# Optimization experiments

Measured on AMD Instinct MI355X. Metric: run time of the kernel, lower is better.

Reference implementation:

```python
import jax, jax.numpy as jnp
import numpy as np

B, S, C_MEL, D_MODEL, K, MAX_DUR = 4, 128, 80, 256, 9, 16
EPS = 1e-5


def setup_inputs():
    key = jax.random.key(0)
    ks = jax.random.split(key, 8)
    rng = np.random.RandomState(0)
    duration = rng.randint(4, MAX_DUR, size=(B, S)).astype(np.int32)
    mel_len = duration.sum(axis=1).astype(np.int32)
    M = int(mel_len.max())
    H = D_MODEL
    def nrm(k, shape, s=0.05):
        return jax.random.normal(k, shape, jnp.float32) * s
    return {
        'mel': jax.random.normal(ks[0], (B, M, C_MEL), jnp.float32),
        'mel_len': jnp.asarray(mel_len),
        'duration': jnp.asarray(duration),
        'src_len': jnp.full((B,), S, dtype=jnp.int32),
        'max_dur': MAX_DUR,
        'conv1_w': nrm(ks[1], (1, K, 1, H), 0.1),
        'bn1_gamma': jnp.ones((H,), jnp.float32),
        'bn1_beta': jnp.zeros((H,), jnp.float32),
        'conv2_w': nrm(ks[2], (1, K, H, 1), 0.05),
        'bn2_gamma': jnp.ones((1,), jnp.float32),
        'bn2_beta': jnp.zeros((1,), jnp.float32),
        'w_ih_f': nrm(ks[3], (3 * H, C_MEL)),
        'w_hh_f': nrm(ks[4], (3 * H, H)),
        'b_ih_f': jnp.zeros((3 * H,), jnp.float32),
        'b_hh_f': jnp.zeros((3 * H,), jnp.float32),
        'w_ih_b': nrm(ks[5], (3 * H, C_MEL)),
        'w_hh_b': nrm(ks[6], (3 * H, H)),
        'b_ih_b': jnp.zeros((3 * H,), jnp.float32),
        'b_hh_b': jnp.zeros((3 * H,), jnp.float32),
    }


def _conv_block(x, w, gamma, beta):
    # x: [N, H=n_mel, W=time, Cin]; conv kernel (1, K) along time, SAME pad, no bias
    p = (w.shape[1] - 1) // 2
    y = jax.lax.conv_general_dilated(x, w, (1, 1), ((0, 0), (p, p)),
                                     dimension_numbers=('NHWC', 'HWIO', 'NHWC'))
    # eval-mode BatchNorm2d (running_mean=0, running_var=1)
    y = y * (gamma / np.sqrt(1.0 + EPS)) + beta
    return jax.nn.relu(y)


def _gru_final(x, mask, w_ih, w_hh, b_ih, b_hh):
    # x: [N, T, C]; mask: [N, T]; returns final hidden state [N, H]
    N, T, _ = x.shape
    H = w_hh.shape[1]
    xg = jnp.einsum('ntc,gc->ntg', x, w_ih) + b_ih  # [N, T, 3H], gates (r,z,n)

    def step(h, inp):
        xg_t, m_t = inp
        hg = h @ w_hh.T + b_hh
        xr, xz, xn = jnp.split(xg_t, 3, axis=-1)
        hr, hz, hn = jnp.split(hg, 3, axis=-1)
        r = jax.nn.sigmoid(xr + hr)
        z = jax.nn.sigmoid(xz + hz)
        n = jnp.tanh(xn + r * hn)
        h_new = (1.0 - z) * n + z * h
        h = jnp.where(m_t[:, None], h_new, h)
        return h, None

    h0 = jnp.zeros((N, H), x.dtype)
    h, _ = jax.lax.scan(step, h0, (xg.swapaxes(0, 1), mask.T))
    return h


def reference(mel, mel_len, duration, src_len, max_dur,
              conv1_w, bn1_gamma, bn1_beta, conv2_w, bn2_gamma, bn2_beta,
              w_ih_f, w_hh_f, b_ih_f, b_hh_f, w_ih_b, w_hh_b, b_ih_b, b_hh_b):
    Bn, M, C = mel.shape
    Sn = duration.shape[1]
    T = max_dur
    t = jnp.arange(T)
    seg_valid = jnp.arange(Sn)[None, :] < src_len[:, None]            # [B, S]
    dur = jnp.where(seg_valid, duration, 0)
    starts = jnp.cumsum(dur, axis=1) - dur                            # [B, S]
    idx = jnp.clip(starts[:, :, None] + t[None, None, :], 0, M - 1)   # [B, S, T]
    mask = t[None, None, :] < dur[:, :, None]                         # [B, S, T]
    segs = jax.vmap(lambda m, i: m[i])(mel, idx.reshape(Bn, -1)).reshape(Bn, Sn, T, C)
    segs = jnp.where(mask[..., None], segs, 0.0)  # zero pad == per-segment conv padding
    N = Bn * Sn
    x = segs.reshape(N, T, C)
    m = mask.reshape(N, T)
    d = dur.reshape(N)
    # conv stack: per mel-channel 1D conv along time, channels 1 -> d_model -> 1
    xc = x.swapaxes(1, 2)[..., None]                                  # [N, C, T, 1]
    xc = _conv_block(xc, conv1_w, bn1_gamma, bn1_beta)                # [N, C, T, D]
    xc = jnp.where(m[:, None, :, None], xc, 0.0)  # restore zero padding between blocks
    xc = _conv_block(xc, conv2_w, bn2_gamma, bn2_beta)                # [N, C, T, 1]
    xg = xc[..., 0].swapaxes(1, 2)                                    # [N, T, C]
    xg = jnp.where(m[..., None], xg, 0.0)
    # bidirectional GRU over each ragged segment; keep only final hidden states
    h_f = _gru_final(xg, m, w_ih_f, w_hh_f, b_ih_f, b_hh_f)
    rev = jnp.clip(d[:, None] - 1 - t[None, :], 0, T - 1)             # reverse within segment
    x_rev = jnp.take_along_axis(xg, rev[..., None], axis=1)
    h_b = _gru_final(x_rev, m, w_ih_b, w_hh_b, b_ih_b, b_hh_b)
    H = w_hh_f.shape[1]
    out = jnp.concatenate([h_f, h_b], axis=-1).reshape(Bn, Sn, 2 * H)
    return jnp.where(seg_valid[..., None], out, 0.0)
```

## Files before the change

kernel.cpp:

```cpp
#include <hip/hip_runtime.h>
#include <hip/hip_bf16.h>
#include <math.h>

#define BB 4
#define SS 128
#define CC 80
#define HH 256
#define KK 9
#define PP 4
#define TT 16
#define NSEG 512
#define G3 768
#define EPSV 1e-5f
#define XKP 96

typedef short bf16x8 __attribute__((ext_vector_type(8)));
typedef float f32x4 __attribute__((ext_vector_type(4)));

#define HSTR 264

__device__ inline ushort f2bf(float f) {
  unsigned x = __float_as_uint(f);
  unsigned r = (x + 0x7FFF + ((x >> 16) & 1)) >> 16;
  return (ushort)r;
}
__device__ inline float fsig(float x) { return 1.f / (1.f + __expf(-x)); }
__device__ inline float ftanh(float x) {
  float e = __expf(2.f * x);
  return 1.f - 2.f / (e + 1.f);
}

__global__ __launch_bounds__(512) void k_prep(const int* __restrict__ duration,
                                              const int* __restrict__ srclen,
                                              int* __restrict__ starts,
                                              int* __restrict__ dur,
                                              int* __restrict__ perm) {
  __shared__ int ds[512];
  __shared__ int hist[17];
  __shared__ int base[17];
  int tid = threadIdx.x;
  int b = tid >> 7, s = tid & 127;
  int v = (s < srclen[b]) ? duration[b * SS + s] : 0;
  ds[tid] = v;
  if (tid < 17) hist[tid] = 0;
  __syncthreads();
  int run = 0;
  for (int s2 = b * 128; s2 < tid; ++s2) run += ds[s2];
  starts[tid] = run;
  dur[tid] = v;
  atomicAdd(&hist[v], 1);
  __syncthreads();
  if (tid == 0) {
    int acc = 0;
    for (int q = 0; q < 17; q++) { base[q] = acc; acc += hist[q]; }
  }
  __syncthreads();
  int rank = atomicAdd(&base[v], 1);
  perm[rank] = tid;
}

__global__ __launch_bounds__(256) void k_wpackc(const float* __restrict__ w1,
                                                const float* __restrict__ g1v,
                                                const float* __restrict__ be1v,
                                                const float* __restrict__ w2,
                                                ushort* __restrict__ wpc) {
  int tid = blockIdx.x * 256 + threadIdx.x;
  if (tid < 8192) {
    int nt = tid >> 9;
    int lane = (tid >> 3) & 63;
    int j = tid & 7;
    int h = nt * 16 + (lane & 15);
    int k = (lane >> 4) * 8 + j;
    float val = 0.f;
    if (k < KK) val = w1[k * HH + h] * (g1v[h] * rsqrtf(1.f + EPSV));
    else if (k == KK) val = be1v[h];
    wpc[tid] = f2bf(val);
  } else if (tid < 12288) {
    int q = tid - 8192;
    int ks = q >> 9;
    int lane = (q >> 3) & 63;
    int j = q & 7;
    int k = lane & 15;
    int h = ks * 32 + (lane >> 4) * 8 + j;
    float val = (k < KK) ? w2[k * HH + h] : 0.f;
    wpc[tid] = f2bf(val);
  }
}

__global__ __launch_bounds__(256) void k_wpackx(const float* __restrict__ wihf,
                                                const float* __restrict__ wihb,
                                                ushort* __restrict__ wpx) {
  int idx = blockIdx.x * 256 + threadIdx.x;
  int j = idx & 7;
  int lane = (idx >> 3) & 63;
  int q = idx >> 9;
  int ks = q % 3;
  int nt = q / 3;
  int n = nt * 16 + (lane & 15);
  int k = ks * 32 + (lane >> 4) * 8 + j;
  float v = 0.f;
  if (k < CC) v = (n < G3) ? wihf[(size_t)n * CC + k]
                           : wihb[(size_t)(n - G3) * CC + k];
  wpx[idx] = f2bf(v);
}

__global__ __launch_bounds__(512, 4) void k_conv(
    const float* __restrict__ mel, const int* __restrict__ starts,
    const int* __restrict__ dur, const ushort* __restrict__ wpc,
    const float* __restrict__ g2v, const float* __restrict__ be2v,
    ushort* __restrict__ xgb, int Mmel) {
  __shared__ __align__(16) ushort xs2[CC][32];
  __shared__ __align__(16) ushort wlc2[4096];
  __shared__ __align__(16) float zs[8][16][18];
  __shared__ __align__(16) float xgs[16][81];

  const int seg = blockIdx.x;
  const int b = seg >> 7;
  const int d = dur[seg];
  const int st = starts[seg];
  const int tid = threadIdx.x;
  const int wv = tid >> 6;
  const int lane = tid & 63;
  const int u = lane & 15;
  const int lgrp = lane >> 4;
  const int hi2 = lgrp >> 1;

  {
    const uint4* src = (const uint4*)(wpc + 8192);
    uint4* dst = (uint4*)wlc2;
    if (tid < 512) dst[tid] = src[tid];
  }
  for (int idx = tid; idx < CC * 16; idx += 512) {
    int c = idx >> 4, t = idx & 15;
    float v = (t < d) ? mel[(size_t)(b * Mmel + st + t) * CC + c] : 0.f;
    xs2[c][t + 4] = f2bf(v);
  }
  for (int idx = tid; idx < CC * 16; idx += 512) {
    int c = idx >> 4, q = idx & 15;
    int p = (q < 4) ? q : (q + 16);
    xs2[c][p] = 0;
  }

  bf16x8 a1r[16];
#pragma unroll
  for (int nt = 0; nt < 16; nt++) {
    a1r[nt] = *(const bf16x8*)&wpc[nt * 512 + lane * 8];
    asm volatile("" : "+v"(a1r[nt]));
  }

  const float g2 = g2v[0] * rsqrtf(1.f + EPSV);
  const float be2 = be2v[0];
  const bool urow = (u < d);
  const unsigned umask = urow ? 0xFFFFFFFFu : 0u;
  const int src0 = (((lane >> 4) & 1) << 5) + u;
  const int src1 = src0 + 16;
  __syncthreads();

#pragma unroll 1
  for (int ci = 0; ci < 10; ci++) {
    const int c = wv * 10 + ci;
    unsigned bw0 = 0, bw1 = 0, bw2 = 0, bw3 = 0;
    if (lgrp == 0) {
      ushort e0 = xs2[c][u + 0], e1 = xs2[c][u + 1];
      ushort e2 = xs2[c][u + 2], e3 = xs2[c][u + 3];
      ushort e4 = xs2[c][u + 4], e5 = xs2[c][u + 5];
      ushort e6 = xs2[c][u + 6], e7 = xs2[c][u + 7];
      bw0 = (unsigned)e0 | ((unsigned)e1 << 16);
      bw1 = (unsigned)e2 | ((unsigned)e3 << 16);
      bw2 = (unsigned)e4 | ((unsigned)e5 << 16);
      bw3 = (unsigned)e6 | ((unsigned)e7 << 16);
    } else if (lgrp == 1) {
      ushort e0 = xs2[c][u + 8];
      bw0 = (unsigned)e0 | (0x3F80u << 16);
    }
    int4 bi4 = make_int4(bw0, bw1, bw2, bw3);
    bf16x8 b1 = *(bf16x8*)&bi4;

    f32x4 accQ = {0.f, 0.f, 0.f, 0.f};

#pragma unroll
    for (int half = 0; half < 2; half++) {
      unsigned P0[8], P1[8];
#pragma unroll
      for (int i = 0; i < 8; i++) {
        f32x4 z = {0.f, 0.f, 0.f, 0.f};
        f32x4 y = __builtin_amdgcn_mfma_f32_16x16x32_bf16(a1r[half * 8 + i],
                                                          b1, z, 0, 0, 0);
        float y0 = fmaxf(y[0], 0.f), y1 = fmaxf(y[1], 0.f);
        float y2 = fmaxf(y[2], 0.f), y3 = fmaxf(y[3], 0.f);
        P0[i] = ((unsigned)__bfloat16_as_ushort(__float2bfloat16(y0)) |
                 ((unsigned)__bfloat16_as_ushort(__float2bfloat16(y1)) << 16)) & umask;
        P1[i] = ((unsigned)__bfloat16_as_ushort(__float2bfloat16(y2)) |
                 ((unsigned)__bfloat16_as_ushort(__float2bfloat16(y3)) << 16)) & umask;
      }
#pragma unroll
      for (int ks2 = 0; ks2 < 4; ks2++) {
        int ks = half * 4 + ks2;
        int v00 = __shfl((int)P0[2 * ks2], src0, 64);
        int v10 = __shfl((int)P0[2 * ks2 + 1], src0, 64);
        unsigned w0 = hi2 ? (unsigned)v10 : (unsigned)v00;
        int v01 = __shfl((int)P1[2 * ks2], src0, 64);
        int v11 = __shfl((int)P1[2 * ks2 + 1], src0, 64);
        unsigned w1 = hi2 ? (unsigned)v11 : (unsigned)v01;
        int v02 = __shfl((int)P0[2 * ks2], src1, 64);
        int v12 = __shfl((int)P0[2 * ks2 + 1], src1, 64);
        unsigned w2 = hi2 ? (unsigned)v12 : (unsigned)v02;
        int v03 = __shfl((int)P1[2 * ks2], src1, 64);
        int v13 = __shfl((int)P1[2 * ks2 + 1], src1, 64);
        unsigned w3 = hi2 ? (unsigned)v13 : (unsigned)v03;
        int4 ai4 = make_int4(w0, w1, w2, w3);
        bf16x8 a2 = *(bf16x8*)&ai4;
        bf16x8 b2 = *(const bf16x8*)&wlc2[ks * 512 + lane * 8];
        accQ = __builtin_amdgcn_mfma_f32_16x16x32_bf16(a2, b2, accQ, 0, 0, 0);
      }
    }

    if (u < KK) {
#pragma unroll
      for (int r = 0; r < 4; r++) zs[wv][lgrp * 4 + r][u] = accQ[r];
    }
    asm volatile("" ::: "memory");

    if (lgrp == 0) {
      float Q = 0.f;
#pragma unroll
      for (int k = 0; k < KK; k++) {
        int idx = u + k - PP;
        if (idx >= 0 && idx < 16) Q += zs[wv][idx][k];
      }
      float qf = urow ? fmaxf(Q * g2 + be2, 0.f) : 0.f;
      xgs[u][c] = qf;
    }
    asm volatile("" ::: "memory");
  }
  __syncthreads();

  for (int idx = tid; idx < 16 * XKP; idx += 512) {
    int t = idx / XKP, kk = idx - t * XKP;
    ushort v = (kk < CC) ? f2bf(xgs[t][kk]) : (ushort)0;
    xgb[(size_t)(seg * TT + t) * XKP + kk] = v;
  }
}

__global__ __launch_bounds__(256) void k_xgate(
    const ushort* __restrict__ xgb, const ushort* __restrict__ wpx,
    const float* __restrict__ bihf, const float* __restrict__ bihb,
    float* __restrict__ G) {
  const int tid = threadIdx.x;
  const int w = tid >> 6, lane = tid & 63;
  const int m0 = blockIdx.x * 64 + w * 16;
  const int by = blockIdx.y;
  const int n0 = by * 64;
  const int lrow = lane & 15, lgrp = lane >> 4;

  bf16x8 a[3];
#pragma unroll
  for (int ks = 0; ks < 3; ks++)
    a[ks] = *(const bf16x8*)&xgb[(size_t)(m0 + lrow) * XKP + ks * 32 + lgrp * 8];

  const float* bsrc = (by < 12) ? bihf : bihb;
  const int nbase = n0 - ((by < 12) ? 0 : G3);

#pragma unroll
  for (int ct = 0; ct < 4; ct++) {
    const int nt = by * 4 + ct;
    f32x4 c = {0.f, 0.f, 0.f, 0.f};
#pragma unroll
    for (int ks = 0; ks < 3; ks++) {
      bf16x8 bfrag = *(const bf16x8*)&wpx[(nt * 3 + ks) * 512 + lane * 8];
      c = __builtin_amdgcn_mfma_f32_16x16x32_bf16(a[ks], bfrag, c, 0, 0, 0);
    }
    float bias = bsrc[nbase + ct * 16 + lrow];
#pragma unroll
    for (int r = 0; r < 4; r++)
      G[(size_t)(m0 + lgrp * 4 + r) * 1536 + n0 + ct * 16 + lrow] = c[r] + bias;
  }
}

__global__ __launch_bounds__(256) void k_wpack(const float* __restrict__ whhf,
                                               const float* __restrict__ whhb,
                                               ushort* __restrict__ wp) {
  int tid = blockIdx.x * 256 + threadIdx.x;
  int r = tid;
  int j = r & 7; r >>= 3;
  int lane = r & 63; r >>= 6;
  int ks = r & 7; r >>= 3;
  int tau = r % 6; r /= 6;
  int wv = r & 7; r >>= 3;
  int dir = r;
  int gate = tau >> 1, a = tau & 1;
  int n = gate * 256 + wv * 32 + a * 16 + (lane & 15);
  int k = ks * 32 + (lane >> 4) * 8 + j;
  float v = (dir ? whhb : whhf)[(size_t)n * HH + k];
  wp[tid] = f2bf(v);
}

__global__ __launch_bounds__(512, 2) void k_gru(
    const float* __restrict__ G, const ushort* __restrict__ wp,
    const float* __restrict__ bhhf, const float* __restrict__ bhhb,
    const int* __restrict__ dur, const int* __restrict__ perm,
    float* __restrict__ out) {
  __shared__ short h_lds[2][16 * HSTR];
  __shared__ ushort wlds[8 * 2 * 8 * 512];
  __shared__ int seg_s[16], d_s[16];

  const int tid = threadIdx.x;
  const int bi = blockIdx.x;
  const int dir = bi >> 5;
  const int grp = bi & 31;
  const int wv = tid >> 6;
  const int lane = tid & 63;
  const int lrow = lane & 15;
  const int lgrp = lane >> 4;

  if (tid < 16) {
    int seg = perm[grp * 16 + tid];
    seg_s[tid] = seg;
    d_s[tid] = dur[seg];
  }
  for (int idx = tid; idx < 2 * 16 * HSTR; idx += 512)
    ((short*)h_lds)[idx] = 0;

  const ushort* wb = wp + (size_t)(dir * 8 + wv) * 6 * 8 * 512 + lane * 8;
  bf16x8 wreg[4][8];
#pragma unroll
  for (int tau = 0; tau < 4; tau++)
#pragma unroll
    for (int ks = 0; ks < 8; ks++)
      wreg[tau][ks] = *(const bf16x8*)&wb[(tau * 8 + ks) * 512];
#pragma unroll
  for (int tt2 = 0; tt2 < 2; tt2++)
#pragma unroll
    for (int ks = 0; ks < 8; ks++) {
      bf16x8 v = *(const bf16x8*)&wb[((4 + tt2) * 8 + ks) * 512];
      *(bf16x8*)&wlds[((wv * 2 + tt2) * 8 + ks) * 512 + lane * 8] = v;
    }
  __syncthreads();

  int d4[4], seg4[4];
#pragma unroll
  for (int r = 0; r < 4; r++) {
    d4[r] = d_s[lgrp * 4 + r];
    seg4[r] = seg_s[lgrp * 4 + r];
  }
  int dmax = 0;
#pragma unroll
  for (int q = 0; q < 16; q++) dmax = max(dmax, d_s[q]);

  const int i0 = wv * 32 + lrow;
  const float* bh = dir ? bhhb : bhhf;
  float bias[3][2];
#pragma unroll
  for (int g = 0; g < 3; g++)
#pragma unroll
    for (int a = 0; a < 2; a++) bias[g][a] = bh[g * 256 + i0 + 16 * a];

  float h[4][2] = {};

  for (int t = 0; t < dmax; t++) {
    const int cur = t & 1;
    float gx[4][3][2];
#pragma unroll
    for (int r = 0; r < 4; r++) {
      if (t < d4[r]) {
        int ts = dir ? (d4[r] - 1 - t) : t;
        const float* grow = G + (size_t)(seg4[r] * TT + ts) * 1536 + dir * G3;
#pragma unroll
        for (int g = 0; g < 3; g++)
#pragma unroll
          for (int a = 0; a < 2; a++) gx[r][g][a] = grow[g * 256 + i0 + 16 * a];
      }
    }
    f32x4 acc[6];
#pragma unroll
    for (int tau = 0; tau < 6; tau++) acc[tau] = (f32x4){0.f, 0.f, 0.f, 0.f};
#pragma unroll
    for (int ks = 0; ks < 8; ks++) {
      bf16x8 av = *(const bf16x8*)&h_lds[cur][lrow * HSTR + ks * 32 + lgrp * 8];
#pragma unroll
      for (int tau = 0; tau < 4; tau++)
        acc[tau] = __builtin_amdgcn_mfma_f32_16x16x32_bf16(av, wreg[tau][ks],
                                                           acc[tau], 0, 0, 0);
#pragma unroll
      for (int tt2 = 0; tt2 < 2; tt2++) {
        bf16x8 wf = *(const bf16x8*)&wlds[((wv * 2 + tt2) * 8 + ks) * 512 + lane * 8];
        acc[4 + tt2] = __builtin_amdgcn_mfma_f32_16x16x32_bf16(av, wf,
                                                               acc[4 + tt2], 0, 0, 0);
      }
    }
#pragma unroll
    for (int r = 0; r < 4; r++) {
      if (t < d4[r]) {
#pragma unroll
        for (int a = 0; a < 2; a++) {
          float rr = fsig(gx[r][0][a] + acc[a][r] + bias[0][a]);
          float zz = fsig(gx[r][1][a] + acc[2 + a][r] + bias[1][a]);
          float nn = ftanh(gx[r][2][a] + rr * (acc[4 + a][r] + bias[2][a]));
          h[r][a] = (1.f - zz) * nn + zz * h[r][a];
          h_lds[cur ^ 1][(lgrp * 4 + r) * HSTR + i0 + 16 * a] = (short)f2bf(h[r][a]);
        }
      }
    }
    __syncthreads();
  }

#pragma unroll
  for (int r = 0; r < 4; r++)
#pragma unroll
    for (int a = 0; a < 2; a++)
      out[(size_t)seg4[r] * 512 + dir * 256 + i0 + 16 * a] = h[r][a];
}

extern "C" void kernel_launch(void* const* d_in, const int* in_sizes, int n_in,
                              void* d_out, int out_size, void* d_ws, size_t ws_size,
                              hipStream_t stream) {
  const float* mel = (const float*)d_in[0];
  const int Mmel = in_sizes[0] / (BB * CC);
  const int* duration = (const int*)d_in[2];
  const int* src_len = (const int*)d_in[3];
  const float* conv1_w = (const float*)d_in[5];
  const float* bn1_g = (const float*)d_in[6];
  const float* bn1_b = (const float*)d_in[7];
  const float* conv2_w = (const float*)d_in[8];
  const float* bn2_g = (const float*)d_in[9];
  const float* bn2_b = (const float*)d_in[10];
  const float* w_ih_f = (const float*)d_in[11];
  const float* w_hh_f = (const float*)d_in[12];
  const float* b_ih_f = (const float*)d_in[13];
  const float* b_hh_f = (const float*)d_in[14];
  const float* w_ih_b = (const float*)d_in[15];
  const float* w_hh_b = (const float*)d_in[16];
  const float* b_ih_b = (const float*)d_in[17];
  const float* b_hh_b = (const float*)d_in[18];

  char* w = (char*)d_ws;
  int* starts = (int*)w;            w += 512 * sizeof(int);
  int* dur = (int*)w;               w += 512 * sizeof(int);
  int* perm = (int*)w;              w += 512 * sizeof(int);
  w += 512 * sizeof(int);
  ushort* xgb = (ushort*)w;         w += (size_t)NSEG * TT * XKP * sizeof(ushort);
  float* G = (float*)w;             w += (size_t)NSEG * TT * 1536 * sizeof(float);
  ushort* wp = (ushort*)w;          w += (size_t)2 * 8 * 6 * 8 * 512 * sizeof(ushort);
  ushort* wpc = (ushort*)w;         w += (size_t)12288 * sizeof(ushort);
  ushort* wpx = (ushort*)w;         w += (size_t)96 * 3 * 512 * sizeof(ushort);
  (void)ws_size; (void)n_in; (void)out_size;

  k_prep<<<1, 512, 0, stream>>>(duration, src_len, starts, dur, perm);
  k_wpack<<<1536, 256, 0, stream>>>(w_hh_f, w_hh_b, wp);
  k_wpackc<<<48, 256, 0, stream>>>(conv1_w, bn1_g, bn1_b, conv2_w, wpc);
  k_wpackx<<<576, 256, 0, stream>>>(w_ih_f, w_ih_b, wpx);
  k_conv<<<NSEG, 512, 0, stream>>>(mel, starts, dur, wpc, bn2_g, bn2_b, xgb, Mmel);
  k_xgate<<<dim3(128, 24), 256, 0, stream>>>(xgb, wpx, b_ih_f, b_ih_b, G);
  k_gru<<<64, 512, 0, stream>>>(G, wp, b_hh_f, b_hh_b, dur, perm, (float*)d_out);
}
```

Baseline: 123.6 us.

## Pre-permute gate rows in k_xgate and prefetch next step gates in GRU

k_xgate now gathers input rows by the GRU's permuted segment order and, for the backward direction, by the time-reversed index. G is therefore laid out exactly in the order the GRU consumes it, so the recurrence can index it with a simple stride. The GRU loop prefetches the next timestep's gate inputs into registers while the current step's MFMAs run, hiding global-load latency on the serial critical path. The cost is more live registers (two gate buffers) and unconditional loads that may read clamped rows past a segment's duration.

Result: no change. 121.7 us (-1.5%).

```diff
diff --git a/kernel.cpp b/kernel.cpp
--- a/kernel.cpp
+++ b/kernel.cpp
@@ -245,6 +245,7 @@
 __global__ __launch_bounds__(256) void k_xgate(
     const ushort* __restrict__ xgb, const ushort* __restrict__ wpx,
     const float* __restrict__ bihf, const float* __restrict__ bihb,
+    const int* __restrict__ dur, const int* __restrict__ perm,
     float* __restrict__ G) {
   const int tid = threadIdx.x;
   const int w = tid >> 6, lane = tid & 63;
@@ -252,14 +253,22 @@
   const int by = blockIdx.y;
   const int n0 = by * 64;
   const int lrow = lane & 15, lgrp = lane >> 4;
+  const int dir = (by < 12) ? 0 : 1;
+
+  const int prank = m0 >> 4;
+  const int seg = perm[prank];
+  const int d = dur[seg];
+  const int t = lrow;
+  int ts = dir ? (d - 1 - t) : t;
+  ts = min(max(ts, 0), TT - 1);
 
   bf16x8 a[3];
 #pragma unroll
   for (int ks = 0; ks < 3; ks++)
-    a[ks] = *(const bf16x8*)&xgb[(size_t)(m0 + lrow) * XKP + ks * 32 + lgrp * 8];
-
-  const float* bsrc = (by < 12) ? bihf : bihb;
-  const int nbase = n0 - ((by < 12) ? 0 : G3);
+    a[ks] = *(const bf16x8*)&xgb[(size_t)(seg * TT + ts) * XKP + ks * 32 + lgrp * 8];
+
+  const float* bsrc = dir ? bihb : bihf;
+  const int nbase = n0 - dir * G3;
 
 #pragma unroll
   for (int ct = 0; ct < 4; ct++) {
@@ -355,22 +364,35 @@
 #pragma unroll
     for (int a = 0; a < 2; a++) bias[g][a] = bh[g * 256 + i0 + 16 * a];
 
+  size_t gbase[4];
+#pragma unroll
+  for (int r = 0; r < 4; r++)
+    gbase[r] = (size_t)((grp * 16 + lgrp * 4 + r) * 16) * 1536 + dir * G3
+               + i0;
+
   float h[4][2] = {};
+  float gxc[4][3][2];
+  float gxn[4][3][2];
+
+#pragma unroll
+  for (int r = 0; r < 4; r++)
+#pragma unroll
+    for (int g = 0; g < 3; g++)
+#pragma unroll
+      for (int a = 0; a < 2; a++)
+        gxc[r][g][a] = G[gbase[r] + g * 256 + 16 * a];
 
   for (int t = 0; t < dmax; t++) {
     const int cur = t & 1;
-    float gx[4][3][2];
-#pragma unroll
-    for (int r = 0; r < 4; r++) {
-      if (t < d4[r]) {
-        int ts = dir ? (d4[r] - 1 - t) : t;
-        const float* grow = G + (size_t)(seg4[r] * TT + ts) * 1536 + dir * G3;
-#pragma unroll
-        for (int g = 0; g < 3; g++)
-#pragma unroll
-          for (int a = 0; a < 2; a++) gx[r][g][a] = grow[g * 256 + i0 + 16 * a];
-      }
-    }
+    const int tn = min(t + 1, TT - 1);
+#pragma unroll
+    for (int r = 0; r < 4; r++)
+#pragma unroll
+      for (int g = 0; g < 3; g++)
+#pragma unroll
+        for (int a = 0; a < 2; a++)
+          gxn[r][g][a] = G[gbase[r] + (size_t)tn * 1536 + g * 256 + 16 * a];
+
     f32x4 acc[6];
 #pragma unroll
     for (int tau = 0; tau < 6; tau++) acc[tau] = (f32x4){0.f, 0.f, 0.f, 0.f};
@@ -393,14 +415,20 @@
       if (t < d4[r]) {
 #pragma unroll
         for (int a = 0; a < 2; a++) {
-          float rr = fsig(gx[r][0][a] + acc[a][r] + bias[0][a]);
-          float zz = fsig(gx[r][1][a] + acc[2 + a][r] + bias[1][a]);
-          float nn = ftanh(gx[r][2][a] + rr * (acc[4 + a][r] + bias[2][a]));
+          float rr = fsig(gxc[r][0][a] + acc[a][r] + bias[0][a]);
+          float zz = fsig(gxc[r][1][a] + acc[2 + a][r] + bias[1][a]);
+          float nn = ftanh(gxc[r][2][a] + rr * (acc[4 + a][r] + bias[2][a]));
           h[r][a] = (1.f - zz) * nn + zz * h[r][a];
           h_lds[cur ^ 1][(lgrp * 4 + r) * HSTR + i0 + 16 * a] = (short)f2bf(h[r][a]);
         }
       }
     }
+#pragma unroll
+    for (int r = 0; r < 4; r++)
+#pragma unroll
+      for (int g = 0; g < 3; g++)
+#pragma unroll
+        for (int a = 0; a < 2; a++) gxc[r][g][a] = gxn[r][g][a];
     __syncthreads();
   }
 
@@ -450,6 +478,6 @@
   k_wpackc<<<48, 256, 0, stream>>>(conv1_w, bn1_g, bn1_b, conv2_w, wpc);
   k_wpackx<<<576, 256, 0, stream>>>(w_ih_f, w_ih_b, wpx);
   k_conv<<<NSEG, 512, 0, stream>>>(mel, starts, dur, wpc, bn2_g, bn2_b, xgb, Mmel);
-  k_xgate<<<dim3(128, 24), 256, 0, stream>>>(xgb, wpx, b_ih_f, b_ih_b, G);
+  k_xgate<<<dim3(128, 24), 256, 0, stream>>>(xgb, wpx, b_ih_f, b_ih_b, dur, perm, G);
   k_gru<<<64, 512, 0, stream>>>(G, wp, b_hh_f, b_hh_b, dur, perm, (float*)d_out);
 }
```
